# Kernel optimization log

Hardware: AMD Instinct MI355X
Metric: run time of the kernel (lower is better)

The kernel has to match this reference:

```python
import jax, jax.numpy as jnp
import numpy as np
import math

FACTOR = 5


def setup_inputs() -> dict:
    key = jax.random.key(0)
    k1, k2, k3, k4 = jax.random.split(key, 4)
    B, L, H, D = 4, 2048, 8, 64
    sample_k = FACTOR * int(np.ceil(np.log(L)))  # 40
    queries = jax.random.normal(k1, (B, L, H, D), dtype=jnp.float32)
    keys = jax.random.normal(k2, (B, L, H, D), dtype=jnp.float32)
    values = jax.random.normal(k3, (B, L, H, D), dtype=jnp.float32)
    # per-query sampled key indices (replaces the host-side random.sample loop)
    index_sample = jax.random.randint(k4, (L, sample_k), 0, L, dtype=jnp.int64)
    return {"queries": queries, "keys": keys, "values": values,
            "index_sample": index_sample}


def reference(queries, keys, values, index_sample):
    B, L_Q, H, D = queries.shape
    L_K = keys.shape[1]
    # [B, L, H, D] -> [B, H, L, D]
    Q = jnp.transpose(queries, (0, 2, 1, 3))
    K = jnp.transpose(keys, (0, 2, 1, 3))
    V = jnp.transpose(values, (0, 2, 1, 3))

    u = min(FACTOR * int(np.ceil(np.log(L_Q))), L_Q)  # n_top

    # --- _prob_QK: sample-score-topk-gather ---
    # K_sample[b,h,i,s,e] = K[b,h,index_sample[i,s],e]  -> [B,H,L_Q,S,E]
    K_sample = K[:, :, index_sample, :]
    Q_K_sample = jnp.einsum('bhie,bhise->bhis', Q, K_sample)  # [B,H,L_Q,S]
    M = Q_K_sample.max(axis=-1) - Q_K_sample.sum(axis=-1) / L_K  # [B,H,L_Q]
    _, M_top = jax.lax.top_k(M, u)  # [B,H,u] indices of sparse queries

    Q_reduce = jnp.take_along_axis(Q, M_top[..., None], axis=2)  # [B,H,u,D]
    scores = jnp.einsum('bhue,bhke->bhuk', Q_reduce, K)  # [B,H,u,L_K]

    scale = 1.0 / math.sqrt(D)
    scores = scores * scale

    # --- initial context (mask_flag=True): causal running sum of V ---
    context = jnp.cumsum(V, axis=2)  # [B,H,L_Q,D]

    # --- ProbMask: causal mask rows gathered at M_top ---
    causal_mask = jnp.arange(L_K)[None, None, None, :] > M_top[..., None]
    scores = jnp.where(causal_mask, -jnp.inf, scores)
    attn = jax.nn.softmax(scores, axis=-1)  # [B,H,u,L_K]

    update = jnp.einsum('bhuk,bhkd->bhud', attn, V)  # [B,H,u,D]
    bi = jnp.arange(B)[:, None, None]
    hi = jnp.arange(H)[None, :, None]
    context = context.at[bi, hi, M_top].set(update)

    # back to [B, L, H, D]
    return jnp.transpose(context, (0, 2, 1, 3))
```

## Files before the change

kernel.cpp:

```cpp
#include <hip/hip_runtime.h>
#include <hip/hip_bf16.h>
#include <math.h>


#define BB 4
#define LL 2048
#define HH 8
#define DD 64
#define SS 40
#define UU 40
#define CC 64
#define LC (LL/CC)

#define KC   64
#define NBIG 8
#define NSUB 4
#define KPAD 68
#define PPAD 68

__global__ void k_measure(const float* __restrict__ Q, const float* __restrict__ K,
                          const int* __restrict__ idx, float* __restrict__ M)
{
    int tid  = threadIdx.x;
    int lane = tid & 63;
    int wave = tid >> 6;
    int qid  = blockIdx.x * 4 + wave;
    int bh = qid / LL;  int i = qid - bh * LL;
    int b  = bh / HH;   int h = bh - b * HH;

    int sg = lane >> 4;
    int d4 = lane & 15;

    const float* qrow = Q + (((size_t)b * LL + i) * HH + h) * DD;
    float4 qv = *(const float4*)(qrow + d4 * 4);

    const float* Kh = K + ((size_t)b * LL * HH + h) * DD;
    const int* ip = idx + (size_t)i * SS;

    float maxv = -INFINITY, sumv = 0.f;
    #pragma unroll
    for (int s0 = 0; s0 < SS; s0 += 4) {
        int kk = ip[s0 + sg];
        const float* krow = Kh + (size_t)kk * (HH * DD);
        float4 kv = *(const float4*)(krow + d4 * 4);
        float p = qv.x * kv.x;
        p = fmaf(qv.y, kv.y, p);
        p = fmaf(qv.z, kv.z, p);
        p = fmaf(qv.w, kv.w, p);
        p += __shfl_xor(p, 1);
        p += __shfl_xor(p, 2);
        p += __shfl_xor(p, 4);
        p += __shfl_xor(p, 8);
        maxv = fmaxf(maxv, p);
        sumv += p;
    }
    maxv = fmaxf(maxv, __shfl_xor(maxv, 16));
    sumv += __shfl_xor(sumv, 16);
    maxv = fmaxf(maxv, __shfl_xor(maxv, 32));
    sumv += __shfl_xor(sumv, 32);

    if (lane == 0) M[qid] = maxv - sumv * (1.0f / (float)LL);
}

__global__ void k_topk(const float* __restrict__ M, int* __restrict__ topIdx)
{
    int lane = threadIdx.x;
    int bh   = blockIdx.x;
    const float* Mp = M + (size_t)bh * LL;

    unsigned k[32];
    #pragma unroll
    for (int r = 0; r < 32; ++r) {
        unsigned u = __float_as_uint(Mp[r * 64 + lane]);
        k[r] = (u & 0x80000000u) ? ~u : (u | 0x80000000u);
    }

    unsigned T = 0u;
    for (int bit = 31; bit >= 0; --bit) {
        unsigned cand = T | (1u << bit);
        int c = 0;
        #pragma unroll
        for (int r = 0; r < 32; ++r) c += (k[r] >= cand) ? 1 : 0;
        #pragma unroll
        for (int off = 1; off < 64; off <<= 1) c += __shfl_xor(c, off);
        if (c >= UU) T = cand;
    }

    int cGT = 0, cGE = 0;
    #pragma unroll
    for (int r = 0; r < 32; ++r) {
        cGT += (k[r] > T) ? 1 : 0;
        cGE += (k[r] >= T) ? 1 : 0;
    }
    #pragma unroll
    for (int off = 1; off < 64; off <<= 1) {
        cGT += __shfl_xor(cGT, off);
        cGE += __shfl_xor(cGE, off);
    }

    int need = UU - cGT;
    int X = LL;
    if (cGE - cGT != need) {
        int lo2 = 0;
        for (int bit = 10; bit >= 0; --bit) {
            int cand = lo2 | (1 << bit);
            int c = 0;
            #pragma unroll
            for (int r = 0; r < 32; ++r)
                c += (k[r] == T && (r * 64 + lane) < cand) ? 1 : 0;
            #pragma unroll
            for (int off = 1; off < 64; off <<= 1) c += __shfl_xor(c, off);
            if (c < need) lo2 = cand;
        }
        X = lo2 + 1;
    }

    unsigned inMask = 0u;
    int cnt = 0;
    #pragma unroll
    for (int r = 0; r < 32; ++r) {
        bool in = (k[r] > T) || (k[r] == T && (r * 64 + lane) < X);
        if (in) { inMask |= 1u << r; ++cnt; }
    }
    int pre = cnt;
    #pragma unroll
    for (int off = 1; off < 64; off <<= 1) {
        int v = __shfl_up(pre, off);
        if (lane >= off) pre += v;
    }
    int slot = pre - cnt;
    #pragma unroll
    for (int r = 0; r < 32; ++r) {
        if ((inMask >> r) & 1u) {
            topIdx[bh * UU + slot] = r * 64 + lane;
            ++slot;
        }
    }
}

__launch_bounds__(256, 1)
__global__ void k_attn_flash(const float* __restrict__ Q, const float* __restrict__ K,
                             const float* __restrict__ V, const int* __restrict__ topIdx,
                             float* __restrict__ mc, float* __restrict__ lc,
                             float* __restrict__ Oc)
{
    __shared__ float sK[KC][KPAD];
    __shared__ float sV[KC][KPAD];
    __shared__ float sP[UU][PPAD];
    __shared__ int   sPos[UU];
    __shared__ float sM[UU], sL[UU], sScale[UU];

    int t   = threadIdx.x;
    int bh  = blockIdx.x / NBIG, big = blockIdx.x % NBIG;
    int b   = bh / HH, h = bh % HH;

    if (t < UU) {
        sPos[t]   = topIdx[bh * UU + t];
        sM[t]     = -INFINITY;
        sL[t]     = 0.f;
    }

    int d4p = t & 15, ug = t >> 4;
    int u0 = ug, u1 = 16 + ug, u2 = 32 + ug;
    int u2c = (u2 < UU) ? u2 : (UU - 1);
    float4 a0 = {0,0,0,0}, a1 = {0,0,0,0}, a2 = {0,0,0,0};

    int j  = t & 63;
    int w  = t >> 6, lane = t & 63;
    int ub = __builtin_amdgcn_readfirstlane(w) * 10;

    for (int sub = 0; sub < NSUB; ++sub) {
        int k0 = (big * NSUB + sub) * KC;
        __syncthreads();

        const float* Kbase = K + (((size_t)b * LL + k0) * HH + h) * DD;
        const float* Vbase = V + (((size_t)b * LL + k0) * HH + h) * DD;
        #pragma unroll
        for (int it = 0; it < 4; ++it) {
            int flat = it * 256 + t;
            int r = flat >> 4, d4 = flat & 15;
            float4 kk = *(const float4*)(Kbase + (size_t)r * (HH * DD) + d4 * 4);
            float4 vv = *(const float4*)(Vbase + (size_t)r * (HH * DD) + d4 * 4);
            *(float4*)&sK[r][d4 * 4] = kk;
            *(float4*)&sV[r][d4 * 4] = vv;
        }
        __syncthreads();

        int jg = k0 + j;
        float kreg[DD];
        #pragma unroll
        for (int d4 = 0; d4 < 16; ++d4) {
            float4 kk = *(const float4*)&sK[j][d4 * 4];
            kreg[d4 * 4 + 0] = kk.x; kreg[d4 * 4 + 1] = kk.y;
            kreg[d4 * 4 + 2] = kk.z; kreg[d4 * 4 + 3] = kk.w;
        }
        #pragma unroll
        for (int iu = 0; iu < 10; iu += 5) {
            int p0 = __builtin_amdgcn_readfirstlane(sPos[ub + iu + 0]);
            int p1 = __builtin_amdgcn_readfirstlane(sPos[ub + iu + 1]);
            int p2 = __builtin_amdgcn_readfirstlane(sPos[ub + iu + 2]);
            int p3 = __builtin_amdgcn_readfirstlane(sPos[ub + iu + 3]);
            int p4 = __builtin_amdgcn_readfirstlane(sPos[ub + iu + 4]);
            const float* q0 = Q + (((size_t)b * LL + p0) * HH + h) * DD;
            const float* q1 = Q + (((size_t)b * LL + p1) * HH + h) * DD;
            const float* q2 = Q + (((size_t)b * LL + p2) * HH + h) * DD;
            const float* q3 = Q + (((size_t)b * LL + p3) * HH + h) * DD;
            const float* q4 = Q + (((size_t)b * LL + p4) * HH + h) * DD;
            float c0 = 0.f, c1 = 0.f, c2 = 0.f, c3 = 0.f, c4 = 0.f;
            #pragma unroll
            for (int d = 0; d < DD; ++d) {
                float kd = kreg[d];
                c0 = fmaf(q0[d], kd, c0);
                c1 = fmaf(q1[d], kd, c1);
                c2 = fmaf(q2[d], kd, c2);
                c3 = fmaf(q3[d], kd, c3);
                c4 = fmaf(q4[d], kd, c4);
            }
            sP[ub + iu + 0][j] = (jg > p0) ? -INFINITY : c0 * 0.125f;
            sP[ub + iu + 1][j] = (jg > p1) ? -INFINITY : c1 * 0.125f;
            sP[ub + iu + 2][j] = (jg > p2) ? -INFINITY : c2 * 0.125f;
            sP[ub + iu + 3][j] = (jg > p3) ? -INFINITY : c3 * 0.125f;
            sP[ub + iu + 4][j] = (jg > p4) ? -INFINITY : c4 * 0.125f;
        }
        __syncthreads();

        for (int i = 0; i < 10; ++i) {
            int u = w * 10 + i;
            float s0 = sP[u][lane];
            float mchunk = s0;
            #pragma unroll
            for (int off = 1; off < 64; off <<= 1)
                mchunk = fmaxf(mchunk, __shfl_xor(mchunk, off));
            float mold = sM[u];
            float mnew = fmaxf(mold, mchunk);
            float e = (mnew == -INFINITY) ? 0.f : __expf(s0 - mnew);
            float lch = e;
            #pragma unroll
            for (int off = 1; off < 64; off <<= 1) lch += __shfl_xor(lch, off);
            float scale = (mold == -INFINITY) ? 0.f : __expf(mold - mnew);
            sP[u][lane] = e;
            if (lane == 0) {
                sM[u] = mnew;
                sL[u] = sL[u] * scale + lch;
                sScale[u] = scale;
            }
        }
        __syncthreads();

        float sc0 = sScale[u0], sc1 = sScale[u1], sc2 = sScale[u2c];
        a0.x *= sc0; a0.y *= sc0; a0.z *= sc0; a0.w *= sc0;
        a1.x *= sc1; a1.y *= sc1; a1.z *= sc1; a1.w *= sc1;
        a2.x *= sc2; a2.y *= sc2; a2.z *= sc2; a2.w *= sc2;
        #pragma unroll 4
        for (int j4 = 0; j4 < KC / 4; ++j4) {
            float4 pj0 = *(const float4*)&sP[u0][j4 * 4];
            float4 pj1 = *(const float4*)&sP[u1][j4 * 4];
            float4 pj2 = *(const float4*)&sP[u2c][j4 * 4];
            float4 va = *(const float4*)&sV[j4 * 4 + 0][d4p * 4];
            float4 vb = *(const float4*)&sV[j4 * 4 + 1][d4p * 4];
            float4 vc = *(const float4*)&sV[j4 * 4 + 2][d4p * 4];
            float4 vd = *(const float4*)&sV[j4 * 4 + 3][d4p * 4];
            a0.x = fmaf(pj0.x, va.x, fmaf(pj0.y, vb.x, fmaf(pj0.z, vc.x, fmaf(pj0.w, vd.x, a0.x))));
            a0.y = fmaf(pj0.x, va.y, fmaf(pj0.y, vb.y, fmaf(pj0.z, vc.y, fmaf(pj0.w, vd.y, a0.y))));
            a0.z = fmaf(pj0.x, va.z, fmaf(pj0.y, vb.z, fmaf(pj0.z, vc.z, fmaf(pj0.w, vd.z, a0.z))));
            a0.w = fmaf(pj0.x, va.w, fmaf(pj0.y, vb.w, fmaf(pj0.z, vc.w, fmaf(pj0.w, vd.w, a0.w))));
            a1.x = fmaf(pj1.x, va.x, fmaf(pj1.y, vb.x, fmaf(pj1.z, vc.x, fmaf(pj1.w, vd.x, a1.x))));
            a1.y = fmaf(pj1.x, va.y, fmaf(pj1.y, vb.y, fmaf(pj1.z, vc.y, fmaf(pj1.w, vd.y, a1.y))));
            a1.z = fmaf(pj1.x, va.z, fmaf(pj1.y, vb.z, fmaf(pj1.z, vc.z, fmaf(pj1.w, vd.z, a1.z))));
            a1.w = fmaf(pj1.x, va.w, fmaf(pj1.y, vb.w, fmaf(pj1.z, vc.w, fmaf(pj1.w, vd.w, a1.w))));
            a2.x = fmaf(pj2.x, va.x, fmaf(pj2.y, vb.x, fmaf(pj2.z, vc.x, fmaf(pj2.w, vd.x, a2.x))));
            a2.y = fmaf(pj2.x, va.y, fmaf(pj2.y, vb.y, fmaf(pj2.z, vc.y, fmaf(pj2.w, vd.y, a2.y))));
            a2.z = fmaf(pj2.x, va.z, fmaf(pj2.y, vb.z, fmaf(pj2.z, vc.z, fmaf(pj2.w, vd.z, a2.z))));
            a2.w = fmaf(pj2.x, va.w, fmaf(pj2.y, vb.w, fmaf(pj2.z, vc.w, fmaf(pj2.w, vd.w, a2.w))));
        }
    }
    __syncthreads();

    int cidx = (bh * NBIG + big) * UU;
    float* ob = Oc + (size_t)cidx * DD;
    *(float4*)&ob[u0 * DD + d4p * 4] = a0;
    *(float4*)&ob[u1 * DD + d4p * 4] = a1;
    if (u2 < UU) *(float4*)&ob[u2 * DD + d4p * 4] = a2;
    if (t < UU) { mc[cidx + t] = sM[t]; lc[cidx + t] = sL[t]; }
}

__global__ void k_combine(const float* __restrict__ mc, const float* __restrict__ lc,
                          const float* __restrict__ Oc, const int* __restrict__ topIdx,
                          float* __restrict__ out)
{
    int bh = blockIdx.x;
    int b  = bh / HH, h = bh % HH;
    int t  = threadIdx.x;
    int d  = t & 63, ug = t >> 6;
    for (int i = 0; i < 10; ++i) {
        int u = ug * 10 + i;
        int pos = topIdx[bh * UU + u];
        float Mx = -INFINITY;
        for (int c = 0; c < NBIG; ++c)
            Mx = fmaxf(Mx, mc[(bh * NBIG + c) * UU + u]);
        float Os = 0.f, Ls = 0.f;
        for (int c = 0; c < NBIG; ++c) {
            int ci = (bh * NBIG + c) * UU + u;
            float m = mc[ci];
            float wgt = (m == -INFINITY) ? 0.f : __expf(m - Mx);
            Ls += wgt * lc[ci];
            Os += wgt * Oc[(size_t)ci * DD + d];
        }
        out[(((size_t)b * LL + pos) * HH + h) * DD + d] = Os / Ls;
    }
}

__global__ void k_chunksum(const float* __restrict__ V, float* __restrict__ chunkSum)
{
    int lane = threadIdx.x;
    int c  = blockIdx.x % CC;
    int bh = blockIdx.x / CC;
    int b  = bh / HH; int h = bh - b * HH;
    float acc = 0.f;
    int l0 = c * LC;
    for (int l = l0; l < l0 + LC; ++l)
        acc += V[(((size_t)b * LL + l) * HH + h) * DD + lane];
    chunkSum[((size_t)bh * CC + c) * DD + lane] = acc;
}

__global__ void k_cumsum(const float* __restrict__ V, const float* __restrict__ chunkSum,
                         float* __restrict__ out)
{
    int lane = threadIdx.x;
    int c  = blockIdx.x % CC;
    int bh = blockIdx.x / CC;
    int b  = bh / HH; int h = bh - b * HH;

    float off = 0.f;
    for (int c2 = 0; c2 < c; ++c2)
        off += chunkSum[((size_t)bh * CC + c2) * DD + lane];

    float acc = off;
    int l0 = c * LC;
    for (int l = l0; l < l0 + LC; ++l) {
        size_t p = (((size_t)b * LL + l) * HH + h) * DD + lane;
        acc += V[p];
        out[p] = acc;
    }
}

extern "C" void kernel_launch(void* const* d_in, const int* in_sizes, int n_in,
                              void* d_out, int out_size, void* d_ws, size_t ws_size,
                              hipStream_t stream)
{
    const float* Q   = (const float*)d_in[0];
    const float* K   = (const float*)d_in[1];
    const float* V   = (const float*)d_in[2];
    const int*   idx = (const int*)d_in[3];
    float* out = (float*)d_out;

    float* M        = (float*)d_ws;
    int*   topIdx   = (int*)(M + (size_t)BB * HH * LL);
    float* mc       = (float*)(topIdx + BB * HH * UU);
    float* lc       = mc + (size_t)BB * HH * NBIG * UU;
    float* Oc       = lc + (size_t)BB * HH * NBIG * UU;
    float* chunkSum = Oc + (size_t)BB * HH * NBIG * UU * DD;

    k_measure   <<<BB * HH * LL / 4, 256, 0, stream>>>(Q, K, idx, M);
    k_topk      <<<BB * HH,           64, 0, stream>>>(M, topIdx);
    k_attn_flash<<<BB * HH * NBIG,   256, 0, stream>>>(Q, K, V, topIdx, mc, lc, Oc);
    k_chunksum  <<<BB * HH * CC,      64, 0, stream>>>(V, chunkSum);
    k_cumsum    <<<BB * HH * CC,      64, 0, stream>>>(V, chunkSum, out);
    k_combine   <<<BB * HH,          256, 0, stream>>>(mc, lc, Oc, topIdx, out);
}
```

Measured before the change: 209.9 us.

## Split attention over key chunks with atomic unnormalized softmax accumulation

The attention kernel now launches one block per 64-key chunk instead of eight blocks per head looping over four chunks. It drops the online max-rescaling and accumulates exp(score) numerators and denominators into global buffers with atomicAdd, which are zeroed inside the measure kernel. A simple finalize kernel divides them. The cumsum and chunksum kernels are also vectorized to float4. Skipping the max subtraction risks overflow for large scores, and the float atomics make summation order nondeterministic.

```diff
diff --git a/kernel.cpp b/kernel.cpp
--- a/kernel.cpp
+++ b/kernel.cpp
@@ -13,15 +13,20 @@
 #define LC (LL/CC)
 
 #define KC   64
-#define NBIG 8
-#define NSUB 4
+#define NCH  (LL/KC)
 #define KPAD 68
 #define PPAD 68
 
+#define NLTOT (BB*HH*UU*DD + BB*HH*UU)
+
 __global__ void k_measure(const float* __restrict__ Q, const float* __restrict__ K,
-                          const int* __restrict__ idx, float* __restrict__ M)
+                          const int* __restrict__ idx, float* __restrict__ M,
+                          float* __restrict__ NL)
 {
     int tid  = threadIdx.x;
+    int gid  = blockIdx.x * 256 + tid;
+    if (gid < NLTOT) NL[gid] = 0.f;
+
     int lane = tid & 63;
     int wave = tid >> 6;
     int qid  = blockIdx.x * 4 + wave;
@@ -138,209 +143,187 @@
     }
 }
 
-__launch_bounds__(256, 1)
-__global__ void k_attn_flash(const float* __restrict__ Q, const float* __restrict__ K,
-                             const float* __restrict__ V, const int* __restrict__ topIdx,
-                             float* __restrict__ mc, float* __restrict__ lc,
-                             float* __restrict__ Oc)
+__launch_bounds__(256, 3)
+__global__ void k_attn(const float* __restrict__ Q, const float* __restrict__ K,
+                       const float* __restrict__ V, const int* __restrict__ topIdx,
+                       float* __restrict__ Ng, float* __restrict__ Lg)
 {
     __shared__ float sK[KC][KPAD];
     __shared__ float sV[KC][KPAD];
     __shared__ float sP[UU][PPAD];
     __shared__ int   sPos[UU];
-    __shared__ float sM[UU], sL[UU], sScale[UU];
-
-    int t   = threadIdx.x;
-    int bh  = blockIdx.x / NBIG, big = blockIdx.x % NBIG;
-    int b   = bh / HH, h = bh % HH;
-
-    if (t < UU) {
-        sPos[t]   = topIdx[bh * UU + t];
-        sM[t]     = -INFINITY;
-        sL[t]     = 0.f;
+
+    int t  = threadIdx.x;
+    int bh = blockIdx.x / NCH, ch = blockIdx.x % NCH;
+    int b  = bh / HH, h = bh % HH;
+    int k0 = ch * KC;
+
+    if (t < UU) sPos[t] = topIdx[bh * UU + t];
+
+    const float* Kbase = K + (((size_t)b * LL + k0) * HH + h) * DD;
+    const float* Vbase = V + (((size_t)b * LL + k0) * HH + h) * DD;
+    #pragma unroll
+    for (int it = 0; it < 4; ++it) {
+        int flat = it * 256 + t;
+        int r = flat >> 4, d4 = flat & 15;
+        float4 kk = *(const float4*)(Kbase + (size_t)r * (HH * DD) + d4 * 4);
+        float4 vv = *(const float4*)(Vbase + (size_t)r * (HH * DD) + d4 * 4);
+        *(float4*)&sK[r][d4 * 4] = kk;
+        *(float4*)&sV[r][d4 * 4] = vv;
+    }
+    __syncthreads();
+
+    int j  = t & 63;
+    int w  = t >> 6, lane = t & 63;
+    int jg = k0 + j;
+    float kreg[DD];
+    #pragma unroll
+    for (int d4 = 0; d4 < 16; ++d4) {
+        float4 kk = *(const float4*)&sK[j][d4 * 4];
+        kreg[d4 * 4 + 0] = kk.x; kreg[d4 * 4 + 1] = kk.y;
+        kreg[d4 * 4 + 2] = kk.z; kreg[d4 * 4 + 3] = kk.w;
+    }
+    int ub = __builtin_amdgcn_readfirstlane(w) * 10;
+
+    #pragma unroll
+    for (int iu = 0; iu < 10; iu += 5) {
+        int p0 = __builtin_amdgcn_readfirstlane(sPos[ub + iu + 0]);
+        int p1 = __builtin_amdgcn_readfirstlane(sPos[ub + iu + 1]);
+        int p2 = __builtin_amdgcn_readfirstlane(sPos[ub + iu + 2]);
+        int p3 = __builtin_amdgcn_readfirstlane(sPos[ub + iu + 3]);
+        int p4 = __builtin_amdgcn_readfirstlane(sPos[ub + iu + 4]);
+        const float* q0 = Q + (((size_t)b * LL + p0) * HH + h) * DD;
+        const float* q1 = Q + (((size_t)b * LL + p1) * HH + h) * DD;
+        const float* q2 = Q + (((size_t)b * LL + p2) * HH + h) * DD;
+        const float* q3 = Q + (((size_t)b * LL + p3) * HH + h) * DD;
+        const float* q4 = Q + (((size_t)b * LL + p4) * HH + h) * DD;
+        float c0 = 0.f, c1 = 0.f, c2 = 0.f, c3 = 0.f, c4 = 0.f;
+        #pragma unroll
+        for (int d = 0; d < DD; ++d) {
+            float kd = kreg[d];
+            c0 = fmaf(q0[d], kd, c0);
+            c1 = fmaf(q1[d], kd, c1);
+            c2 = fmaf(q2[d], kd, c2);
+            c3 = fmaf(q3[d], kd, c3);
+            c4 = fmaf(q4[d], kd, c4);
+        }
+        sP[ub + iu + 0][j] = (jg > p0) ? 0.f : __expf(c0 * 0.125f);
+        sP[ub + iu + 1][j] = (jg > p1) ? 0.f : __expf(c1 * 0.125f);
+        sP[ub + iu + 2][j] = (jg > p2) ? 0.f : __expf(c2 * 0.125f);
+        sP[ub + iu + 3][j] = (jg > p3) ? 0.f : __expf(c3 * 0.125f);
+        sP[ub + iu + 4][j] = (jg > p4) ? 0.f : __expf(c4 * 0.125f);
+    }
+    __syncthreads();
+
+    for (int i = 0; i < 10; ++i) {
+        int u = w * 10 + i;
+        float e = sP[u][lane];
+        #pragma unroll
+        for (int off = 1; off < 64; off <<= 1) e += __shfl_xor(e, off);
+        if (lane == 0) atomicAdd(&Lg[bh * UU + u], e);
     }
 
     int d4p = t & 15, ug = t >> 4;
     int u0 = ug, u1 = 16 + ug, u2 = 32 + ug;
     int u2c = (u2 < UU) ? u2 : (UU - 1);
     float4 a0 = {0,0,0,0}, a1 = {0,0,0,0}, a2 = {0,0,0,0};
-
-    int j  = t & 63;
-    int w  = t >> 6, lane = t & 63;
-    int ub = __builtin_amdgcn_readfirstlane(w) * 10;
-
-    for (int sub = 0; sub < NSUB; ++sub) {
-        int k0 = (big * NSUB + sub) * KC;
-        __syncthreads();
-
-        const float* Kbase = K + (((size_t)b * LL + k0) * HH + h) * DD;
-        const float* Vbase = V + (((size_t)b * LL + k0) * HH + h) * DD;
-        #pragma unroll
-        for (int it = 0; it < 4; ++it) {
-            int flat = it * 256 + t;
-            int r = flat >> 4, d4 = flat & 15;
-            float4 kk = *(const float4*)(Kbase + (size_t)r * (HH * DD) + d4 * 4);
-            float4 vv = *(const float4*)(Vbase + (size_t)r * (HH * DD) + d4 * 4);
-            *(float4*)&sK[r][d4 * 4] = kk;
-            *(float4*)&sV[r][d4 * 4] = vv;
-        }
-        __syncthreads();
-
-        int jg = k0 + j;
-        float kreg[DD];
-        #pragma unroll
-        for (int d4 = 0; d4 < 16; ++d4) {
-            float4 kk = *(const float4*)&sK[j][d4 * 4];
-            kreg[d4 * 4 + 0] = kk.x; kreg[d4 * 4 + 1] = kk.y;
-            kreg[d4 * 4 + 2] = kk.z; kreg[d4 * 4 + 3] = kk.w;
-        }
-        #pragma unroll
-        for (int iu = 0; iu < 10; iu += 5) {
-            int p0 = __builtin_amdgcn_readfirstlane(sPos[ub + iu + 0]);
-            int p1 = __builtin_amdgcn_readfirstlane(sPos[ub + iu + 1]);
-            int p2 = __builtin_amdgcn_readfirstlane(sPos[ub + iu + 2]);
-            int p3 = __builtin_amdgcn_readfirstlane(sPos[ub + iu + 3]);
-            int p4 = __builtin_amdgcn_readfirstlane(sPos[ub + iu + 4]);
-            const float* q0 = Q + (((size_t)b * LL + p0) * HH + h) * DD;
-            const float* q1 = Q + (((size_t)b * LL + p1) * HH + h) * DD;
-            const float* q2 = Q + (((size_t)b * LL + p2) * HH + h) * DD;
-            const float* q3 = Q + (((size_t)b * LL + p3) * HH + h) * DD;
-            const float* q4 = Q + (((size_t)b * LL + p4) * HH + h) * DD;
-            float c0 = 0.f, c1 = 0.f, c2 = 0.f, c3 = 0.f, c4 = 0.f;
-            #pragma unroll
-            for (int d = 0; d < DD; ++d) {
-                float kd = kreg[d];
-                c0 = fmaf(q0[d], kd, c0);
-                c1 = fmaf(q1[d], kd, c1);
-                c2 = fmaf(q2[d], kd, c2);
-                c3 = fmaf(q3[d], kd, c3);
-                c4 = fmaf(q4[d], kd, c4);
-            }
-            sP[ub + iu + 0][j] = (jg > p0) ? -INFINITY : c0 * 0.125f;
-            sP[ub + iu + 1][j] = (jg > p1) ? -INFINITY : c1 * 0.125f;
-            sP[ub + iu + 2][j] = (jg > p2) ? -INFINITY : c2 * 0.125f;
-            sP[ub + iu + 3][j] = (jg > p3) ? -INFINITY : c3 * 0.125f;
-            sP[ub + iu + 4][j] = (jg > p4) ? -INFINITY : c4 * 0.125f;
-        }
-        __syncthreads();
-
-        for (int i = 0; i < 10; ++i) {
-            int u = w * 10 + i;
-            float s0 = sP[u][lane];
-            float mchunk = s0;
-            #pragma unroll
-            for (int off = 1; off < 64; off <<= 1)
-                mchunk = fmaxf(mchunk, __shfl_xor(mchunk, off));
-            float mold = sM[u];
-            float mnew = fmaxf(mold, mchunk);
-            float e = (mnew == -INFINITY) ? 0.f : __expf(s0 - mnew);
-            float lch = e;
-            #pragma unroll
-            for (int off = 1; off < 64; off <<= 1) lch += __shfl_xor(lch, off);
-            float scale = (mold == -INFINITY) ? 0.f : __expf(mold - mnew);
-            sP[u][lane] = e;
-            if (lane == 0) {
-                sM[u] = mnew;
-                sL[u] = sL[u] * scale + lch;
-                sScale[u] = scale;
-            }
-        }
-        __syncthreads();
-
-        float sc0 = sScale[u0], sc1 = sScale[u1], sc2 = sScale[u2c];
-        a0.x *= sc0; a0.y *= sc0; a0.z *= sc0; a0.w *= sc0;
-        a1.x *= sc1; a1.y *= sc1; a1.z *= sc1; a1.w *= sc1;
-        a2.x *= sc2; a2.y *= sc2; a2.z *= sc2; a2.w *= sc2;
-        #pragma unroll 4
-        for (int j4 = 0; j4 < KC / 4; ++j4) {
-            float4 pj0 = *(const float4*)&sP[u0][j4 * 4];
-            float4 pj1 = *(const float4*)&sP[u1][j4 * 4];
-            float4 pj2 = *(const float4*)&sP[u2c][j4 * 4];
-            float4 va = *(const float4*)&sV[j4 * 4 + 0][d4p * 4];
-            float4 vb = *(const float4*)&sV[j4 * 4 + 1][d4p * 4];
-            float4 vc = *(const float4*)&sV[j4 * 4 + 2][d4p * 4];
-            float4 vd = *(const float4*)&sV[j4 * 4 + 3][d4p * 4];
-            a0.x = fmaf(pj0.x, va.x, fmaf(pj0.y, vb.x, fmaf(pj0.z, vc.x, fmaf(pj0.w, vd.x, a0.x))));
-            a0.y = fmaf(pj0.x, va.y, fmaf(pj0.y, vb.y, fmaf(pj0.z, vc.y, fmaf(pj0.w, vd.y, a0.y))));
-            a0.z = fmaf(pj0.x, va.z, fmaf(pj0.y, vb.z, fmaf(pj0.z, vc.z, fmaf(pj0.w, vd.z, a0.z))));
-            a0.w = fmaf(pj0.x, va.w, fmaf(pj0.y, vb.w, fmaf(pj0.z, vc.w, fmaf(pj0.w, vd.w, a0.w))));
-            a1.x = fmaf(pj1.x, va.x, fmaf(pj1.y, vb.x, fmaf(pj1.z, vc.x, fmaf(pj1.w, vd.x, a1.x))));
-            a1.y = fmaf(pj1.x, va.y, fmaf(pj1.y, vb.y, fmaf(pj1.z, vc.y, fmaf(pj1.w, vd.y, a1.y))));
-            a1.z = fmaf(pj1.x, va.z, fmaf(pj1.y, vb.z, fmaf(pj1.z, vc.z, fmaf(pj1.w, vd.z, a1.z))));
-            a1.w = fmaf(pj1.x, va.w, fmaf(pj1.y, vb.w, fmaf(pj1.z, vc.w, fmaf(pj1.w, vd.w, a1.w))));
-            a2.x = fmaf(pj2.x, va.x, fmaf(pj2.y, vb.x, fmaf(pj2.z, vc.x, fmaf(pj2.w, vd.x, a2.x))));
-            a2.y = fmaf(pj2.x, va.y, fmaf(pj2.y, vb.y, fmaf(pj2.z, vc.y, fmaf(pj2.w, vd.y, a2.y))));
-            a2.z = fmaf(pj2.x, va.z, fmaf(pj2.y, vb.z, fmaf(pj2.z, vc.z, fmaf(pj2.w, vd.z, a2.z))));
-            a2.w = fmaf(pj2.x, va.w, fmaf(pj2.y, vb.w, fmaf(pj2.z, vc.w, fmaf(pj2.w, vd.w, a2.w))));
-        }
-    }
-    __syncthreads();
-
-    int cidx = (bh * NBIG + big) * UU;
-    float* ob = Oc + (size_t)cidx * DD;
-    *(float4*)&ob[u0 * DD + d4p * 4] = a0;
-    *(float4*)&ob[u1 * DD + d4p * 4] = a1;
-    if (u2 < UU) *(float4*)&ob[u2 * DD + d4p * 4] = a2;
-    if (t < UU) { mc[cidx + t] = sM[t]; lc[cidx + t] = sL[t]; }
-}
-
-__global__ void k_combine(const float* __restrict__ mc, const float* __restrict__ lc,
-                          const float* __restrict__ Oc, const int* __restrict__ topIdx,
-                          float* __restrict__ out)
+    #pragma unroll 4
+    for (int j4 = 0; j4 < KC / 4; ++j4) {
+        float4 pj0 = *(const float4*)&sP[u0][j4 * 4];
+        float4 pj1 = *(const float4*)&sP[u1][j4 * 4];
+        float4 pj2 = *(const float4*)&sP[u2c][j4 * 4];
+        float4 va = *(const float4*)&sV[j4 * 4 + 0][d4p * 4];
+        float4 vb = *(const float4*)&sV[j4 * 4 + 1][d4p * 4];
+        float4 vc = *(const float4*)&sV[j4 * 4 + 2][d4p * 4];
+        float4 vd = *(const float4*)&sV[j4 * 4 + 3][d4p * 4];
+        a0.x = fmaf(pj0.x, va.x, fmaf(pj0.y, vb.x, fmaf(pj0.z, vc.x, fmaf(pj0.w, vd.x, a0.x))));
+        a0.y = fmaf(pj0.x, va.y, fmaf(pj0.y, vb.y, fmaf(pj0.z, vc.y, fmaf(pj0.w, vd.y, a0.y))));
+        a0.z = fmaf(pj0.x, va.z, fmaf(pj0.y, vb.z, fmaf(pj0.z, vc.z, fmaf(pj0.w, vd.z, a0.z))));
+        a0.w = fmaf(pj0.x, va.w, fmaf(pj0.y, vb.w, fmaf(pj0.z, vc.w, fmaf(pj0.w, vd.w, a0.w))));
+        a1.x = fmaf(pj1.x, va.x, fmaf(pj1.y, vb.x, fmaf(pj1.z, vc.x, fmaf(pj1.w, vd.x, a1.x))));
+        a1.y = fmaf(pj1.x, va.y, fmaf(pj1.y, vb.y, fmaf(pj1.z, vc.y, fmaf(pj1.w, vd.y, a1.y))));
+        a1.z = fmaf(pj1.x, va.z, fmaf(pj1.y, vb.z, fmaf(pj1.z, vc.z, fmaf(pj1.w, vd.z, a1.z))));
+        a1.w = fmaf(pj1.x, va.w, fmaf(pj1.y, vb.w, fmaf(pj1.z, vc.w, fmaf(pj1.w, vd.w, a1.w))));
+        a2.x = fmaf(pj2.x, va.x, fmaf(pj2.y, vb.x, fmaf(pj2.z, vc.x, fmaf(pj2.w, vd.x, a2.x))));
+        a2.y = fmaf(pj2.x, va.y, fmaf(pj2.y, vb.y, fmaf(pj2.z, vc.y, fmaf(pj2.w, vd.y, a2.y))));
+        a2.z = fmaf(pj2.x, va.z, fmaf(pj2.y, vb.z, fmaf(pj2.z, vc.z, fmaf(pj2.w, vd.z, a2.z))));
+        a2.w = fmaf(pj2.x, va.w, fmaf(pj2.y, vb.w, fmaf(pj2.z, vc.w, fmaf(pj2.w, vd.w, a2.w))));
+    }
+
+    float* n0 = Ng + ((size_t)(bh * UU + u0) * DD + d4p * 4);
+    float* n1 = Ng + ((size_t)(bh * UU + u1) * DD + d4p * 4);
+    atomicAdd(n0 + 0, a0.x); atomicAdd(n0 + 1, a0.y);
+    atomicAdd(n0 + 2, a0.z); atomicAdd(n0 + 3, a0.w);
+    atomicAdd(n1 + 0, a1.x); atomicAdd(n1 + 1, a1.y);
+    atomicAdd(n1 + 2, a1.z); atomicAdd(n1 + 3, a1.w);
+    if (u2 < UU) {
+        float* n2 = Ng + ((size_t)(bh * UU + u2) * DD + d4p * 4);
+        atomicAdd(n2 + 0, a2.x); atomicAdd(n2 + 1, a2.y);
+        atomicAdd(n2 + 2, a2.z); atomicAdd(n2 + 3, a2.w);
+    }
+}
+
+__global__ void k_chunksum(const float* __restrict__ V, float* __restrict__ chunkSum)
+{
+    int t  = threadIdx.x;
+    int c  = blockIdx.x % CC;
+    int bh = blockIdx.x / CC;
+    int b  = bh / HH; int h = bh - b * HH;
+    int d4 = t & 15, rs = t >> 4;
+
+    float4 acc = {0,0,0,0};
+    int l0 = c * LC;
+    for (int l = l0 + rs; l < l0 + LC; l += 4) {
+        float4 v = *(const float4*)(V + (((size_t)b * LL + l) * HH + h) * DD + d4 * 4);
+        acc.x += v.x; acc.y += v.y; acc.z += v.z; acc.w += v.w;
+    }
+    acc.x += __shfl_xor(acc.x, 16); acc.y += __shfl_xor(acc.y, 16);
+    acc.z += __shfl_xor(acc.z, 16); acc.w += __shfl_xor(acc.w, 16);
+    acc.x += __shfl_xor(acc.x, 32); acc.y += __shfl_xor(acc.y, 32);
+    acc.z += __shfl_xor(acc.z, 32); acc.w += __shfl_xor(acc.w, 32);
+    if (t < 16)
+        *(float4*)(chunkSum + ((size_t)bh * CC + c) * DD + d4 * 4) = acc;
+}
+
+__global__ void k_cumsum(const float* __restrict__ V, const float* __restrict__ chunkSum,
+                         float* __restrict__ out)
+{
+    int t  = threadIdx.x;
+    int bh = blockIdx.x / (CC / 4);
+    int cg = blockIdx.x % (CC / 4);
+    int b  = bh / HH; int h = bh - b * HH;
+    int d4 = t & 15;
+    int c  = cg * 4 + (t >> 4);
+
+    const float4* CS4 = (const float4*)chunkSum;
+    float4 acc = {0,0,0,0};
+    for (int c2 = 0; c2 < c; ++c2) {
+        float4 s = CS4[((size_t)bh * CC + c2) * 16 + d4];
+        acc.x += s.x; acc.y += s.y; acc.z += s.z; acc.w += s.w;
+    }
+
+    int l0 = c * LC;
+    for (int l = l0; l < l0 + LC; ++l) {
+        size_t p = (((size_t)b * LL + l) * HH + h) * DD + d4 * 4;
+        float4 v = *(const float4*)(V + p);
+        acc.x += v.x; acc.y += v.y; acc.z += v.z; acc.w += v.w;
+        *(float4*)(out + p) = acc;
+    }
+}
+
+__global__ void k_finalize(const float* __restrict__ Ng, const float* __restrict__ Lg,
+                           const int* __restrict__ topIdx, float* __restrict__ out)
 {
     int bh = blockIdx.x;
     int b  = bh / HH, h = bh % HH;
     int t  = threadIdx.x;
-    int d  = t & 63, ug = t >> 6;
+    int d  = t & 63, w = t >> 6;
     for (int i = 0; i < 10; ++i) {
-        int u = ug * 10 + i;
+        int u = w * 10 + i;
         int pos = topIdx[bh * UU + u];
-        float Mx = -INFINITY;
-        for (int c = 0; c < NBIG; ++c)
-            Mx = fmaxf(Mx, mc[(bh * NBIG + c) * UU + u]);
-        float Os = 0.f, Ls = 0.f;
-        for (int c = 0; c < NBIG; ++c) {
-            int ci = (bh * NBIG + c) * UU + u;
-            float m = mc[ci];
-            float wgt = (m == -INFINITY) ? 0.f : __expf(m - Mx);
-            Ls += wgt * lc[ci];
-            Os += wgt * Oc[(size_t)ci * DD + d];
-        }
-        out[(((size_t)b * LL + pos) * HH + h) * DD + d] = Os / Ls;
-    }
-}
-
-__global__ void k_chunksum(const float* __restrict__ V, float* __restrict__ chunkSum)
-{
-    int lane = threadIdx.x;
-    int c  = blockIdx.x % CC;
-    int bh = blockIdx.x / CC;
-    int b  = bh / HH; int h = bh - b * HH;
-    float acc = 0.f;
-    int l0 = c * LC;
-    for (int l = l0; l < l0 + LC; ++l)
-        acc += V[(((size_t)b * LL + l) * HH + h) * DD + lane];
-    chunkSum[((size_t)bh * CC + c) * DD + lane] = acc;
-}
-
-__global__ void k_cumsum(const float* __restrict__ V, const float* __restrict__ chunkSum,
-                         float* __restrict__ out)
-{
-    int lane = threadIdx.x;
-    int c  = blockIdx.x % CC;
-    int bh = blockIdx.x / CC;
-    int b  = bh / HH; int h = bh - b * HH;
-
-    float off = 0.f;
-    for (int c2 = 0; c2 < c; ++c2)
-        off += chunkSum[((size_t)bh * CC + c2) * DD + lane];
-
-    float acc = off;
-    int l0 = c * LC;
-    for (int l = l0; l < l0 + LC; ++l) {
-        size_t p = (((size_t)b * LL + l) * HH + h) * DD + lane;
-        acc += V[p];
-        out[p] = acc;
+        float num = Ng[((size_t)bh * UU + u) * DD + d];
+        float den = Lg[bh * UU + u];
+        out[(((size_t)b * LL + pos) * HH + h) * DD + d] = num / den;
     }
 }
 
@@ -356,15 +339,14 @@
 
     float* M        = (float*)d_ws;
     int*   topIdx   = (int*)(M + (size_t)BB * HH * LL);
-    float* mc       = (float*)(topIdx + BB * HH * UU);
-    float* lc       = mc + (size_t)BB * HH * NBIG * UU;
-    float* Oc       = lc + (size_t)BB * HH * NBIG * UU;
-    float* chunkSum = Oc + (size_t)BB * HH * NBIG * UU * DD;
-
-    k_measure   <<<BB * HH * LL / 4, 256, 0, stream>>>(Q, K, idx, M);
-    k_topk      <<<BB * HH,           64, 0, stream>>>(M, topIdx);
-    k_attn_flash<<<BB * HH * NBIG,   256, 0, stream>>>(Q, K, V, topIdx, mc, lc, Oc);
-    k_chunksum  <<<BB * HH * CC,      64, 0, stream>>>(V, chunkSum);
-    k_cumsum    <<<BB * HH * CC,      64, 0, stream>>>(V, chunkSum, out);
-    k_combine   <<<BB * HH,          256, 0, stream>>>(mc, lc, Oc, topIdx, out);
-}
+    float* Ng       = (float*)(topIdx + BB * HH * UU);
+    float* Lg       = Ng + (size_t)BB * HH * UU * DD;
+    float* chunkSum = Lg + BB * HH * UU;
+
+    k_measure <<<BB * HH * LL / 4, 256, 0, stream>>>(Q, K, idx, M, Ng);
+    k_topk    <<<BB * HH,           64, 0, stream>>>(M, topIdx);
+    k_attn    <<<BB * HH * NCH,    256, 0, stream>>>(Q, K, V, topIdx, Ng, Lg);
+    k_chunksum<<<BB * HH * CC,      64, 0, stream>>>(V, chunkSum);
+    k_cumsum  <<<BB * HH * (CC/4),  64, 0, stream>>>(V, chunkSum, out);
+    k_finalize<<<BB * HH,          256, 0, stream>>>(Ng, Lg, topIdx, out);
+}
```

After: 233.5 us. 11.2% more time.
